# Kernel tuning notes

Hardware: AMD Instinct MI355X
Metric: run time of the kernel (lower is better)

The kernel has to match this reference:

```python
import jax, jax.numpy as jnp
import numpy as np

D = 1024
H = 16
HD = D // H  # 64
HIDDEN = ((int(D * 8 / 3) + 63) // 64) * 64  # 2752
EPS = 1e-6


def rmsnorm(x, w):
    rms = jnp.sqrt(jnp.mean(x * x, axis=-1, keepdims=True) + EPS)
    return x / rms * w


def setup_inputs() -> dict:
    key = jax.random.key(0)
    ks = jax.random.split(key, 12)
    s = lambda fan_in: 1.0 / np.sqrt(fan_in)
    return {
        "x": jax.random.normal(ks[0], (4, 16, 256, D), dtype=jnp.float32),
        "time_emb": jax.random.normal(ks[1], (4, D), dtype=jnp.float32),
        "norm1_w": jnp.ones((D,), dtype=jnp.float32),
        "norm2_w": jnp.ones((D,), dtype=jnp.float32),
        # weights stored (in, out), i.e. transpose of torch nn.Linear.weight
        "qkv_w": jax.random.normal(ks[2], (D, 3 * H * HD), dtype=jnp.float32) * s(D),
        "out_w": jax.random.normal(ks[3], (H * HD, D), dtype=jnp.float32) * s(H * HD),
        "w1": jax.random.normal(ks[4], (D, HIDDEN), dtype=jnp.float32) * s(D),
        "w2": jax.random.normal(ks[5], (D, HIDDEN), dtype=jnp.float32) * s(D),
        "w3": jax.random.normal(ks[6], (HIDDEN, D), dtype=jnp.float32) * s(HIDDEN),
        "mod_w": jax.random.normal(ks[7], (D, 6 * D), dtype=jnp.float32) * s(D),
        "mod_b": jnp.zeros((6 * D,), dtype=jnp.float32),
    }


def spatial_attention(h, qkv_w, out_w):
    # h: (B, T, S, D); attention over S independently per (B, T)
    B, T, S, _ = h.shape
    qkv = jnp.einsum('btsd,de->btse', h, qkv_w)  # (B,T,S,3*H*HD)
    qkv = qkv.reshape(B, T, S, 3, H, HD)
    q, k, v = qkv[..., 0, :, :], qkv[..., 1, :, :], qkv[..., 2, :, :]  # (B,T,S,H,HD)
    scale = HD ** -0.5
    scores = jnp.einsum('btqhd,btkhd->bthqk', q, k) * scale  # (B,T,H,S,S)
    attn = jax.nn.softmax(scores, axis=-1)
    out = jnp.einsum('bthqk,btkhd->btqhd', attn, v).reshape(B, T, S, H * HD)
    return jnp.einsum('btse,ed->btsd', out, out_w)


def reference(x, time_emb, norm1_w, norm2_w, qkv_w, out_w, w1, w2, w3, mod_w, mod_b):
    # adaLN modulation from (B, D) time_emb -> broadcast over (T, S)
    mod = jax.nn.silu(time_emb) @ mod_w + mod_b  # (B, 6D)
    mod = mod[:, None, None, :]  # (B,1,1,6D)
    shift1, scale1, gate1, shift2, scale2, gate2 = jnp.split(mod, 6, axis=-1)

    h = rmsnorm(x, norm1_w) * (1.0 + scale1) + shift1
    h = spatial_attention(h, qkv_w, out_w)
    x = x + gate1 * h

    h = rmsnorm(x, norm2_w) * (1.0 + scale2) + shift2
    h = (jax.nn.silu(h @ w1) * (h @ w2)) @ w3  # SwiGLU
    x = x + gate2 * h
    return x
```

## Files before the change

kernel.cpp:

```cpp
#include <hip/hip_runtime.h>
#include <stdint.h>


using bf16x8 = __attribute__((ext_vector_type(8))) short;
using f32x4  = __attribute__((ext_vector_type(4))) float;

typedef __attribute__((address_space(3))) uint16_t lds16_t;

__device__ __forceinline__ float bf2f(uint16_t h) {
  union { uint32_t u; float f; } v; v.u = ((uint32_t)h) << 16; return v.f;
}
__device__ __forceinline__ uint16_t f2bf(float f) {
  union { float f; uint32_t u; } v; v.f = f;
  uint32_t r = v.u + 0x7FFFu + ((v.u >> 16) & 1u);
  return (uint16_t)(r >> 16);
}
__device__ __forceinline__ float silu(float x) { return x / (1.0f + __expf(-x)); }

__device__ __forceinline__ void gload16(const uint16_t* g, lds16_t* l) {
  __builtin_amdgcn_global_load_lds(
      (const __attribute__((address_space(1))) void*)g,
      (__attribute__((address_space(3))) void*)l, 16, 0, 0);
}

__global__ __launch_bounds__(256)
void transpose_cast(const float* __restrict__ w, uint16_t* __restrict__ wt,
                    int K, int N) {
  __shared__ float tile[32][33];
  int n0 = blockIdx.x * 32, k0 = blockIdx.y * 32;
  int tx = threadIdx.x & 31, ty = threadIdx.x >> 5;
#pragma unroll
  for (int it = 0; it < 4; ++it) {
    int r = ty + it * 8;
    tile[r][tx] = w[(k0 + r) * N + n0 + tx];
  }
  __syncthreads();
#pragma unroll
  for (int it = 0; it < 4; ++it) {
    int r = ty + it * 8;
    wt[(n0 + r) * K + k0 + tx] = f2bf(tile[tx][r]);
  }
}

__global__ __launch_bounds__(1024)
void mod_kernel(const float* __restrict__ te, const float* __restrict__ mw,
                const float* __restrict__ mb, float* __restrict__ mod) {
  __shared__ float ste[4096];
  __shared__ float red[4][4][256];
  int tid = threadIdx.x;
  for (int i = tid; i < 4096; i += 1024) { float v = te[i]; ste[i] = silu(v); }
  __syncthreads();
  int kslice = tid >> 8, cl = tid & 255;
  int col = blockIdx.x * 256 + cl;
  float acc[4] = {0.f, 0.f, 0.f, 0.f};
  for (int kk = 0; kk < 256; ++kk) {
    int k = kslice * 256 + kk;
    float wv = mw[k * 6144 + col];
#pragma unroll
    for (int b = 0; b < 4; ++b) acc[b] += ste[b * 1024 + k] * wv;
  }
#pragma unroll
  for (int b = 0; b < 4; ++b) red[kslice][b][cl] = acc[b];
  __syncthreads();
  if (kslice == 0) {
#pragma unroll
    for (int b = 0; b < 4; ++b)
      mod[b * 6144 + col] =
          red[0][b][cl] + red[1][b][cl] + red[2][b][cl] + red[3][b][cl] + mb[col];
  }
}

__global__ __launch_bounds__(256)
void norm_kernel(const float* __restrict__ xf,
                 const float* __restrict__ w, const float* __restrict__ mod,
                 int shift_off, int scale_off, uint16_t* __restrict__ out) {
  int row = blockIdx.x;
  int b = row >> 12;
  int tid = threadIdx.x;
  float4 t = *(const float4*)(xf + (size_t)row * 1024 + tid * 4);
  float v[4] = {t.x, t.y, t.z, t.w};
  float ss = v[0] * v[0] + v[1] * v[1] + v[2] * v[2] + v[3] * v[3];
#pragma unroll
  for (int off = 1; off < 64; off <<= 1) ss += __shfl_xor(ss, off);
  __shared__ float red[4];
  if ((tid & 63) == 0) red[tid >> 6] = ss;
  __syncthreads();
  float tot = red[0] + red[1] + red[2] + red[3];
  float rinv = rsqrtf(tot * (1.0f / 1024.0f) + 1e-6f);
  const float* mrow = mod + b * 6144;
  uint16_t o[4];
#pragma unroll
  for (int c = 0; c < 4; ++c) {
    int col = tid * 4 + c;
    float hv = v[c] * rinv * w[col] * (1.0f + mrow[scale_off + col]) + mrow[shift_off + col];
    o[c] = f2bf(hv);
  }
  uint2 pk;
  pk.x = (uint32_t)o[0] | ((uint32_t)o[1] << 16);
  pk.y = (uint32_t)o[2] | ((uint32_t)o[3] << 16);
  *(uint2*)(out + (size_t)row * 1024 + tid * 4) = pk;
}

template <int MODE>
__global__ __launch_bounds__(256)
void gemm_bt(const uint16_t* __restrict__ A, const uint16_t* __restrict__ Bt,
             int M, int N, int K,
             uint16_t* __restrict__ obf,
             const float* __restrict__ xin, const float* __restrict__ mod,
             const uint16_t* __restrict__ h1, float* __restrict__ xio) {
  __shared__ uint16_t As[2][128 * 64];
  __shared__ uint16_t Bs[2][128 * 64];
  const int tiles_n = (N + 127) >> 7;
  const int xcd = blockIdx.x & 7;
  const int slot = blockIdx.x >> 3;
  const int tm = (slot / tiles_n) * 8 + xcd;
  const int tn = slot % tiles_n;
  const int m0 = tm * 128, n0 = tn * 128;
  const int tid = threadIdx.x;
  const int wave = tid >> 6, lane = tid & 63;
  const int wm = (wave & 1) * 64, wn = (wave >> 1) * 64;
  const int col = lane & 15, quad = lane >> 4;

  const int srow = tid >> 3, sphys = tid & 7;
  const int slog = ((sphys ^ (srow & 7)) << 3);
  const uint16_t* Ag[4]; const uint16_t* Bg[4];
#pragma unroll
  for (int r = 0; r < 4; ++r) {
    Ag[r] = A + (size_t)(m0 + 32 * r + srow) * K + slog;
    int br = n0 + 32 * r + srow; if (br >= N) br = N - 1;
    Bg[r] = Bt + (size_t)br * K + slog;
  }
  lds16_t* Alb[2]; lds16_t* Blb[2];
#pragma unroll
  for (int b = 0; b < 2; ++b) {
    Alb[b] = (lds16_t*)As[b] + tid * 8;
    Blb[b] = (lds16_t*)Bs[b] + tid * 8;
  }

  f32x4 acc[4][4];
#pragma unroll
  for (int i = 0; i < 4; ++i)
#pragma unroll
    for (int j = 0; j < 4; ++j) acc[i][j] = (f32x4){0.f, 0.f, 0.f, 0.f};

  const int c7 = col & 7;
  const int swzk[2] = {((quad ^ c7) << 3), (((4 + quad) ^ c7) << 3)};

#pragma unroll
  for (int r = 0; r < 4; ++r) gload16(Ag[r], Alb[0] + r * 2048);
#pragma unroll
  for (int r = 0; r < 4; ++r) gload16(Bg[r], Blb[0] + r * 2048);

  for (int k0 = 0; k0 < K; k0 += 64) {
    const int cur = (k0 >> 6) & 1;
    __syncthreads();
    if (k0 + 64 < K) {
      const int kn = k0 + 64;
#pragma unroll
      for (int r = 0; r < 4; ++r) gload16(Ag[r] + kn, Alb[cur ^ 1] + r * 2048);
#pragma unroll
      for (int r = 0; r < 4; ++r) gload16(Bg[r] + kn, Blb[cur ^ 1] + r * 2048);
    }
    const uint16_t* Ab = As[cur];
    const uint16_t* Bb = Bs[cur];
#pragma unroll
    for (int ks = 0; ks < 2; ++ks) {
      const int swz = swzk[ks];
      bf16x8 af[4], bfr[4];
#pragma unroll
      for (int i = 0; i < 4; ++i)
        af[i] = *(const bf16x8*)(Ab + (wm + i * 16 + col) * 64 + swz);
#pragma unroll
      for (int j = 0; j < 4; ++j)
        bfr[j] = *(const bf16x8*)(Bb + (wn + j * 16 + col) * 64 + swz);
#pragma unroll
      for (int i = 0; i < 4; ++i)
#pragma unroll
        for (int j = 0; j < 4; ++j)
          acc[i][j] = __builtin_amdgcn_mfma_f32_16x16x32_bf16(af[i], bfr[j], acc[i][j], 0, 0, 0);
    }
  }

#pragma unroll
  for (int i = 0; i < 4; ++i) {
#pragma unroll
    for (int j = 0; j < 4; ++j) {
#pragma unroll
      for (int r = 0; r < 4; ++r) {
        int row = m0 + wm + i * 16 + quad * 4 + r;
        int cn = n0 + wn + j * 16 + col;
        if (cn >= N) continue;
        float c = acc[i][j][r];
        if (MODE == 0) {
          obf[(size_t)row * N + cn] = f2bf(c);
        } else if (MODE == 1) {
          int b = row >> 12;
          size_t idx = (size_t)row * 1024 + cn;
          float g = mod[b * 6144 + 2048 + cn];
          xio[idx] = xin[idx] + g * c;
        } else if (MODE == 2) {
          obf[(size_t)row * N + cn] = f2bf(silu(c));
        } else if (MODE == 3) {
          size_t idx = (size_t)row * N + cn;
          obf[idx] = f2bf(bf2f(h1[idx]) * c);
        } else {
          int b = row >> 12;
          size_t idx = (size_t)row * 1024 + cn;
          float g = mod[b * 6144 + 5120 + cn];
          xio[idx] = xio[idx] + g * c;
        }
      }
    }
  }
}

__global__ __launch_bounds__(256)
void attn_kernel(const uint16_t* __restrict__ qkv, uint16_t* __restrict__ out) {
  __shared__ uint16_t lds[32768];
  const int tid = threadIdx.x;
  const int bid = blockIdx.x;
  const int slice = bid >> 2, qc = bid & 3;
  const int bt = slice >> 4, h = slice & 15;
  const int row0 = bt * 256;
  const int wave = tid >> 6, lane = tid & 63;
  const int col = lane & 15, quad = lane >> 4;

  {
    int kr = tid;
    const uint16_t* kp = qkv + (size_t)(row0 + kr) * 3072 + 1024 + h * 64;
    uint16_t* ks = lds + kr * 64;
#pragma unroll
    for (int kc = 0; kc < 8; ++kc) {
      uint4 v = *(const uint4*)(kp + kc * 8);
      *(uint4*)(ks + ((kc ^ (kr & 7)) << 3)) = v;
    }
  }
  {
    int p = tid & 127, dh = tid >> 7;
    const uint16_t* vp0 = qkv + (size_t)(row0 + 2 * p) * 3072 + 2048 + h * 64 + dh * 32;
    const uint16_t* vp1 = vp0 + 3072;
    uint16_t r0[32], r1[32];
#pragma unroll
    for (int i = 0; i < 4; ++i) {
      *(uint4*)(r0 + i * 8) = *(const uint4*)(vp0 + i * 8);
      *(uint4*)(r1 + i * 8) = *(const uint4*)(vp1 + i * 8);
    }
    uint32_t* vt = (uint32_t*)(lds + 16384);
    int krc = p >> 2;
#pragma unroll
    for (int i = 0; i < 32; ++i) {
      int d = dh * 32 + i;
      uint32_t val = (uint32_t)r0[i] | ((uint32_t)r1[i] << 16);
      vt[d * 128 + ((krc ^ (d & 7)) << 2) + (p & 3)] = val;
    }
  }
  __syncthreads();

  const int qrow = qc * 64 + wave * 16 + col;
  const uint16_t* qp = qkv + (size_t)(row0 + qrow) * 3072 + h * 64;
  bf16x8 aq0 = *(const bf16x8*)(qp + quad * 8);
  bf16x8 aq1 = *(const bf16x8*)(qp + 32 + quad * 8);

  f32x4 sc[16];
#pragma unroll
  for (int t = 0; t < 16; ++t) {
    int n = t * 16 + col;
    const uint16_t* kb = lds + n * 64;
    bf16x8 b0 = *(const bf16x8*)(kb + ((quad ^ (n & 7)) << 3));
    bf16x8 b1 = *(const bf16x8*)(kb + (((4 + quad) ^ (n & 7)) << 3));
    f32x4 s = (f32x4){0.f, 0.f, 0.f, 0.f};
    s = __builtin_amdgcn_mfma_f32_16x16x32_bf16(aq0, b0, s, 0, 0, 0);
    s = __builtin_amdgcn_mfma_f32_16x16x32_bf16(aq1, b1, s, 0, 0, 0);
    sc[t] = s;
  }

  const float scale = 0.125f;
  float inv[4];
#pragma unroll
  for (int i = 0; i < 4; ++i) {
    float m = -1e30f;
#pragma unroll
    for (int t = 0; t < 16; ++t) m = fmaxf(m, sc[t][i]);
    m = fmaxf(m, __shfl_xor(m, 1));
    m = fmaxf(m, __shfl_xor(m, 2));
    m = fmaxf(m, __shfl_xor(m, 4));
    m = fmaxf(m, __shfl_xor(m, 8));
    m *= scale;
    float sum = 0.f;
#pragma unroll
    for (int t = 0; t < 16; ++t) {
      float p = __expf(sc[t][i] * scale - m);
      sc[t][i] = p;
      sum += p;
    }
    sum += __shfl_xor(sum, 1);
    sum += __shfl_xor(sum, 2);
    sum += __shfl_xor(sum, 4);
    sum += __shfl_xor(sum, 8);
    inv[i] = 1.0f / sum;
  }
  __syncthreads();

  uint16_t* P = lds + wave * 4096;
#pragma unroll
  for (int t = 0; t < 16; ++t) {
    int pcb = t * 2 + (col >> 3);
#pragma unroll
    for (int i = 0; i < 4; ++i) {
      int r = quad * 4 + i;
      P[r * 256 + ((pcb ^ (r & 7)) << 3) + (col & 7)] = f2bf(sc[t][i] * inv[i]);
    }
  }

  f32x4 o[4];
#pragma unroll
  for (int nt = 0; nt < 4; ++nt) o[nt] = (f32x4){0.f, 0.f, 0.f, 0.f};
  const uint16_t* Vt = lds + 16384;
#pragma unroll
  for (int c = 0; c < 8; ++c) {
    int pc = c * 4 + quad;
    bf16x8 ap = *(const bf16x8*)(P + col * 256 + ((pc ^ (col & 7)) << 3));
#pragma unroll
    for (int nt = 0; nt < 4; ++nt) {
      int d = nt * 16 + col;
      bf16x8 bv = *(const bf16x8*)(Vt + d * 256 + ((pc ^ (d & 7)) << 3));
      o[nt] = __builtin_amdgcn_mfma_f32_16x16x32_bf16(ap, bv, o[nt], 0, 0, 0);
    }
  }

#pragma unroll
  for (int nt = 0; nt < 4; ++nt) {
#pragma unroll
    for (int r = 0; r < 4; ++r) {
      int grow = row0 + qc * 64 + wave * 16 + quad * 4 + r;
      int gcol = h * 64 + nt * 16 + col;
      out[(size_t)grow * 1024 + gcol] = f2bf(o[nt][r]);
    }
  }
}

extern "C" void kernel_launch(void* const* d_in, const int* in_sizes, int n_in,
                              void* d_out, int out_size, void* d_ws, size_t ws_size,
                              hipStream_t stream) {
  const float* x        = (const float*)d_in[0];
  const float* time_emb = (const float*)d_in[1];
  const float* norm1_w  = (const float*)d_in[2];
  const float* norm2_w  = (const float*)d_in[3];
  const float* qkv_w    = (const float*)d_in[4];
  const float* out_w    = (const float*)d_in[5];
  const float* w1       = (const float*)d_in[6];
  const float* w2       = (const float*)d_in[7];
  const float* w3       = (const float*)d_in[8];
  const float* mod_w    = (const float*)d_in[9];
  const float* mod_b    = (const float*)d_in[10];
  float* out = (float*)d_out;

  char* ws = (char*)d_ws;
  float*    mod    = (float*)(ws);
  uint16_t* wqkv_t = (uint16_t*)(ws + 98304);
  uint16_t* wout_t = (uint16_t*)(ws + 6389760);
  uint16_t* w1t    = (uint16_t*)(ws + 8486912);
  uint16_t* w2t    = (uint16_t*)(ws + 14123008);
  uint16_t* w3t    = (uint16_t*)(ws + 19759104);
  uint16_t* hbuf   = (uint16_t*)(ws + 25395200);
  uint16_t* qkvb   = (uint16_t*)(ws + 58949632);
  uint16_t* hid    = qkvb;

  dim3 blk(256);
  transpose_cast<<<dim3(3072 / 32, 1024 / 32), blk, 0, stream>>>(qkv_w, wqkv_t, 1024, 3072);
  transpose_cast<<<dim3(1024 / 32, 1024 / 32), blk, 0, stream>>>(out_w, wout_t, 1024, 1024);
  transpose_cast<<<dim3(2752 / 32, 1024 / 32), blk, 0, stream>>>(w1, w1t, 1024, 2752);
  transpose_cast<<<dim3(2752 / 32, 1024 / 32), blk, 0, stream>>>(w2, w2t, 1024, 2752);
  transpose_cast<<<dim3(1024 / 32, 2752 / 32), blk, 0, stream>>>(w3, w3t, 2752, 1024);

  mod_kernel<<<24, 1024, 0, stream>>>(time_emb, mod_w, mod_b, mod);

  norm_kernel<<<16384, blk, 0, stream>>>(x, norm1_w, mod, 0, 1024, hbuf);

  gemm_bt<0><<<128 * 24, blk, 0, stream>>>(hbuf, wqkv_t, 16384, 3072, 1024,
                                           qkvb, nullptr, nullptr, nullptr, nullptr);
  attn_kernel<<<4096, blk, 0, stream>>>(qkvb, hbuf);

  gemm_bt<1><<<128 * 8, blk, 0, stream>>>(hbuf, wout_t, 16384, 1024, 1024,
                                          nullptr, x, mod, nullptr, out);
  norm_kernel<<<16384, blk, 0, stream>>>(out, norm2_w, mod, 3072, 4096, hbuf);

  gemm_bt<2><<<128 * 22, blk, 0, stream>>>(hbuf, w1t, 16384, 2752, 1024,
                                           hid, nullptr, nullptr, nullptr, nullptr);
  gemm_bt<3><<<128 * 22, blk, 0, stream>>>(hbuf, w2t, 16384, 2752, 1024,
                                           hid, nullptr, nullptr, hid, nullptr);
  gemm_bt<4><<<128 * 8, blk, 0, stream>>>(hid, w3t, 16384, 1024, 2752,
                                          nullptr, nullptr, mod, nullptr, out);
}
```

Before: 825.3 us.

## Replace 128x128 GEMM with 256x256-tile 8-wave pipelined GEMM and padded hidden dim

Replaces the 128x128, 4-wave GEMM with a 256x256-tile, 8-wave kernel. Global-to-LDS loads are interleaved between MFMA groups using explicit barriers, waitcnt and setprio scheduling. The SwiGLU hidden dimension is padded from 2752 to 2816, with zero-filled weight buffers, so N and K are multiples of 256/64 and the bounds checks go away. The aim is more data reuse per tile and better overlap of memory and matrix work. The cost is extra memsets, padded compute and heavier register and LDS use per block, which lowers occupancy.

Result: slower. 861.9 us (+4.4%).

```diff
diff --git a/kernel.cpp b/kernel.cpp
--- a/kernel.cpp
+++ b/kernel.cpp
@@ -25,20 +25,20 @@
 
 __global__ __launch_bounds__(256)
 void transpose_cast(const float* __restrict__ w, uint16_t* __restrict__ wt,
-                    int K, int N) {
+                    int K, int N, int ldt) {
   __shared__ float tile[32][33];
   int n0 = blockIdx.x * 32, k0 = blockIdx.y * 32;
   int tx = threadIdx.x & 31, ty = threadIdx.x >> 5;
 #pragma unroll
   for (int it = 0; it < 4; ++it) {
     int r = ty + it * 8;
-    tile[r][tx] = w[(k0 + r) * N + n0 + tx];
+    tile[r][tx] = w[(size_t)(k0 + r) * N + n0 + tx];
   }
   __syncthreads();
 #pragma unroll
   for (int it = 0; it < 4; ++it) {
     int r = ty + it * 8;
-    wt[(n0 + r) * K + k0 + tx] = f2bf(tile[tx][r]);
+    wt[(size_t)(n0 + r) * ldt + k0 + tx] = f2bf(tile[tx][r]);
   }
 }
 
@@ -101,107 +101,161 @@
   *(uint2*)(out + (size_t)row * 1024 + tid * 4) = pk;
 }
 
+
+#define BAR __builtin_amdgcn_s_barrier()
+#define LGKM0                                            \
+  do {                                                   \
+    asm volatile("s_waitcnt lgkmcnt(0)" ::: "memory");   \
+    __builtin_amdgcn_sched_barrier(0);                   \
+  } while (0)
+#define VMW(N) asm volatile("s_waitcnt vmcnt(" #N ")" ::: "memory")
+
+#define GRD4(DST, BASE, ROWB, SWZ)                                           \
+  {                                                                          \
+    _Pragma("unroll") for (int q_ = 0; q_ < 4; ++q_)                         \
+        DST[q_] = *(const bf16x8*)((BASE) + ((ROWB) + q_ * 16 + col) * 64 +  \
+                                   (SWZ));                                   \
+  }
+
+#define MM16(I0, AF)                                                         \
+  {                                                                          \
+    __builtin_amdgcn_s_setprio(1);                                           \
+    _Pragma("unroll") for (int q_ = 0; q_ < 4; ++q_) {                       \
+      _Pragma("unroll") for (int j_ = 0; j_ < 4; ++j_)                       \
+          acc[(I0) + q_][j_] = __builtin_amdgcn_mfma_f32_16x16x32_bf16(      \
+              AF[q_], bf[j_], acc[(I0) + q_][j_], 0, 0, 0);                  \
+    }                                                                        \
+    __builtin_amdgcn_s_setprio(0);                                           \
+  }
+
+#define ADST(S, H, G) ((lds16_t*)As[(S)] + (H) * 8192 + (G) * 4096 + sdoff)
+#define BDST(S, H, G) ((lds16_t*)Bs[(S)] + (H) * 8192 + (G) * 4096 + sdoff)
+
+#define TILE(S, KA, KB, DO_A, DO_B, VMTAIL)                                  \
+  {                                                                          \
+    bf16x8 af[4], bf[4];                                                     \
+                                                                \
+    GRD4(af, As[S], wm * 128, swz0);                                         \
+    GRD4(bf, Bs[S], wn * 64, swz0);                                          \
+    if (DO_A) {                                                              \
+      gload16(aS00 + (KA), ADST((S) ^ 1, 0, 0));                             \
+      gload16(aS01 + (KA), ADST((S) ^ 1, 0, 1));                             \
+    }                                                                        \
+    BAR; LGKM0;                                                              \
+    MM16(0, af);                                                             \
+    BAR;                                                                     \
+                                                                \
+    GRD4(af, As[S], wm * 128 + 64, swz0);                                    \
+    if (DO_A) {                                                              \
+      gload16(aS10 + (KA), ADST((S) ^ 1, 1, 0));                             \
+      gload16(aS11 + (KA), ADST((S) ^ 1, 1, 1));                             \
+    }                                                                        \
+    BAR; LGKM0;                                                              \
+    MM16(4, af);                                                             \
+    BAR;                                                                     \
+                                                                \
+    GRD4(af, As[S], wm * 128, swz1);                                         \
+    GRD4(bf, Bs[S], wn * 64, swz1);                                          \
+    BAR; LGKM0;                                                              \
+    MM16(0, af);                                                             \
+    BAR;                                                                     \
+                                                                \
+    GRD4(af, As[S], wm * 128 + 64, swz1);                                    \
+    if (DO_B) {                                                              \
+      gload16(bS00 + (KB), BDST(S, 0, 0));                                   \
+      gload16(bS01 + (KB), BDST(S, 0, 1));                                   \
+      gload16(bS10 + (KB), BDST(S, 1, 0));                                   \
+      gload16(bS11 + (KB), BDST(S, 1, 1));                                   \
+    }                                                                        \
+    BAR; LGKM0;                                                              \
+    MM16(4, af);                                                             \
+    VMTAIL;                                                                  \
+    BAR;                                                                     \
+  }
+
 template <int MODE>
-__global__ __launch_bounds__(256)
-void gemm_bt(const uint16_t* __restrict__ A, const uint16_t* __restrict__ Bt,
-             int M, int N, int K,
-             uint16_t* __restrict__ obf,
-             const float* __restrict__ xin, const float* __restrict__ mod,
-             const uint16_t* __restrict__ h1, float* __restrict__ xio) {
-  __shared__ uint16_t As[2][128 * 64];
-  __shared__ uint16_t Bs[2][128 * 64];
-  const int tiles_n = (N + 127) >> 7;
+__global__ __launch_bounds__(512)
+void gemm256(const uint16_t* __restrict__ A, int lda,
+             const uint16_t* __restrict__ Bt, int ldb,
+             int N, int K, int ldc,
+             uint16_t* __restrict__ obf, const float* __restrict__ xin,
+             const float* __restrict__ mod, const uint16_t* __restrict__ h1,
+             float* __restrict__ xio) {
+  __shared__ uint16_t As[2][16384];
+  __shared__ uint16_t Bs[2][16384];
+  const int tiles_n = N >> 8;
   const int xcd = blockIdx.x & 7;
-  const int slot = blockIdx.x >> 3;
-  const int tm = (slot / tiles_n) * 8 + xcd;
-  const int tn = slot % tiles_n;
-  const int m0 = tm * 128, n0 = tn * 128;
+  const int bslot = blockIdx.x >> 3;
+  const int tm = (bslot / tiles_n) * 8 + xcd;
+  const int tn = bslot % tiles_n;
+  const int m0 = tm * 256, n0 = tn * 256;
   const int tid = threadIdx.x;
   const int wave = tid >> 6, lane = tid & 63;
-  const int wm = (wave & 1) * 64, wn = (wave >> 1) * 64;
+  const int wm = wave >> 2, wn = wave & 3;
   const int col = lane & 15, quad = lane >> 4;
-
-  const int srow = tid >> 3, sphys = tid & 7;
-  const int slog = ((sphys ^ (srow & 7)) << 3);
-  const uint16_t* Ag[4]; const uint16_t* Bg[4];
-#pragma unroll
-  for (int r = 0; r < 4; ++r) {
-    Ag[r] = A + (size_t)(m0 + 32 * r + srow) * K + slog;
-    int br = n0 + 32 * r + srow; if (br >= N) br = N - 1;
-    Bg[r] = Bt + (size_t)br * K + slog;
-  }
-  lds16_t* Alb[2]; lds16_t* Blb[2];
-#pragma unroll
-  for (int b = 0; b < 2; ++b) {
-    Alb[b] = (lds16_t*)As[b] + tid * 8;
-    Blb[b] = (lds16_t*)Bs[b] + tid * 8;
-  }
-
-  f32x4 acc[4][4];
-#pragma unroll
-  for (int i = 0; i < 4; ++i)
+  const int c7 = col & 7;
+  const int swz0 = (quad ^ c7) << 3;
+  const int swz1 = ((4 + quad) ^ c7) << 3;
+  const int sdoff = wave * 512 + lane * 8;
+
+  const int srl = lane >> 3;
+  const int sl8 = ((lane & 7) ^ srl) << 3;
+  const int rg0 = wave * 8 + srl;
+  const int rg1 = 64 + wave * 8 + srl;
+  const uint16_t* aS00 = A + (size_t)(m0 + rg0) * lda + sl8;
+  const uint16_t* aS01 = A + (size_t)(m0 + rg1) * lda + sl8;
+  const uint16_t* aS10 = A + (size_t)(m0 + 128 + rg0) * lda + sl8;
+  const uint16_t* aS11 = A + (size_t)(m0 + 128 + rg1) * lda + sl8;
+  const uint16_t* bS00 = Bt + (size_t)(n0 + rg0) * ldb + sl8;
+  const uint16_t* bS01 = Bt + (size_t)(n0 + rg1) * ldb + sl8;
+  const uint16_t* bS10 = Bt + (size_t)(n0 + 128 + rg0) * ldb + sl8;
+  const uint16_t* bS11 = Bt + (size_t)(n0 + 128 + rg1) * ldb + sl8;
+
+  f32x4 acc[8][4];
+#pragma unroll
+  for (int i = 0; i < 8; ++i)
 #pragma unroll
     for (int j = 0; j < 4; ++j) acc[i][j] = (f32x4){0.f, 0.f, 0.f, 0.f};
 
-  const int c7 = col & 7;
-  const int swzk[2] = {((quad ^ c7) << 3), (((4 + quad) ^ c7) << 3)};
-
-#pragma unroll
-  for (int r = 0; r < 4; ++r) gload16(Ag[r], Alb[0] + r * 2048);
-#pragma unroll
-  for (int r = 0; r < 4; ++r) gload16(Bg[r], Blb[0] + r * 2048);
-
-  for (int k0 = 0; k0 < K; k0 += 64) {
-    const int cur = (k0 >> 6) & 1;
-    __syncthreads();
-    if (k0 + 64 < K) {
-      const int kn = k0 + 64;
-#pragma unroll
-      for (int r = 0; r < 4; ++r) gload16(Ag[r] + kn, Alb[cur ^ 1] + r * 2048);
-#pragma unroll
-      for (int r = 0; r < 4; ++r) gload16(Bg[r] + kn, Blb[cur ^ 1] + r * 2048);
-    }
-    const uint16_t* Ab = As[cur];
-    const uint16_t* Bb = Bs[cur];
-#pragma unroll
-    for (int ks = 0; ks < 2; ++ks) {
-      const int swz = swzk[ks];
-      bf16x8 af[4], bfr[4];
-#pragma unroll
-      for (int i = 0; i < 4; ++i)
-        af[i] = *(const bf16x8*)(Ab + (wm + i * 16 + col) * 64 + swz);
-#pragma unroll
-      for (int j = 0; j < 4; ++j)
-        bfr[j] = *(const bf16x8*)(Bb + (wn + j * 16 + col) * 64 + swz);
-#pragma unroll
-      for (int i = 0; i < 4; ++i)
-#pragma unroll
-        for (int j = 0; j < 4; ++j)
-          acc[i][j] = __builtin_amdgcn_mfma_f32_16x16x32_bf16(af[i], bfr[j], acc[i][j], 0, 0, 0);
-    }
-  }
-
-#pragma unroll
-  for (int i = 0; i < 4; ++i) {
+  gload16(bS00, BDST(0, 0, 0)); gload16(bS01, BDST(0, 0, 1));
+  gload16(bS10, BDST(0, 1, 0)); gload16(bS11, BDST(0, 1, 1));
+  gload16(aS00, ADST(0, 0, 0)); gload16(aS01, ADST(0, 0, 1));
+  gload16(aS10, ADST(0, 1, 0)); gload16(aS11, ADST(0, 1, 1));
+  gload16(bS00 + 64, BDST(1, 0, 0)); gload16(bS01 + 64, BDST(1, 0, 1));
+  gload16(bS10 + 64, BDST(1, 1, 0)); gload16(bS11 + 64, BDST(1, 1, 1));
+  VMW(4);
+  BAR;
+
+  const int NT = K >> 6;
+  int k0 = 0;
+  for (int t = 0; t + 2 < NT; t += 2) {
+    TILE(0, k0 + 64, k0 + 128, true, true, VMW(4));
+    TILE(1, k0 + 128, k0 + 192, true, true, VMW(4));
+    k0 += 128;
+  }
+  TILE(0, k0 + 64, 0, true, false, VMW(0));
+  TILE(1, 0, 0, false, false, (void)0);
+
+#pragma unroll
+  for (int i = 0; i < 8; ++i) {
 #pragma unroll
     for (int j = 0; j < 4; ++j) {
 #pragma unroll
       for (int r = 0; r < 4; ++r) {
-        int row = m0 + wm + i * 16 + quad * 4 + r;
-        int cn = n0 + wn + j * 16 + col;
-        if (cn >= N) continue;
+        int row = m0 + wm * 128 + i * 16 + quad * 4 + r;
+        int cn = n0 + wn * 64 + j * 16 + col;
         float c = acc[i][j][r];
         if (MODE == 0) {
-          obf[(size_t)row * N + cn] = f2bf(c);
+          obf[(size_t)row * ldc + cn] = f2bf(c);
         } else if (MODE == 1) {
           int b = row >> 12;
           size_t idx = (size_t)row * 1024 + cn;
           float g = mod[b * 6144 + 2048 + cn];
           xio[idx] = xin[idx] + g * c;
         } else if (MODE == 2) {
-          obf[(size_t)row * N + cn] = f2bf(silu(c));
+          obf[(size_t)row * ldc + cn] = f2bf(silu(c));
         } else if (MODE == 3) {
-          size_t idx = (size_t)row * N + cn;
+          size_t idx = (size_t)row * ldc + cn;
           obf[idx] = f2bf(bf2f(h1[idx]) * c);
         } else {
           int b = row >> 12;
@@ -360,35 +414,39 @@
   uint16_t* wqkv_t = (uint16_t*)(ws + 98304);
   uint16_t* wout_t = (uint16_t*)(ws + 6389760);
   uint16_t* w1t    = (uint16_t*)(ws + 8486912);
-  uint16_t* w2t    = (uint16_t*)(ws + 14123008);
-  uint16_t* w3t    = (uint16_t*)(ws + 19759104);
-  uint16_t* hbuf   = (uint16_t*)(ws + 25395200);
-  uint16_t* qkvb   = (uint16_t*)(ws + 58949632);
+  uint16_t* w2t    = (uint16_t*)(ws + 14254080);
+  uint16_t* w3t    = (uint16_t*)(ws + 20021248);
+  uint16_t* hbuf   = (uint16_t*)(ws + 25788416);
+  uint16_t* qkvb   = (uint16_t*)(ws + 59342848);
   uint16_t* hid    = qkvb;
 
+  hipMemsetAsync(w1t, 0, (size_t)2816 * 1024 * 2, stream);
+  hipMemsetAsync(w2t, 0, (size_t)2816 * 1024 * 2, stream);
+  hipMemsetAsync(w3t, 0, (size_t)1024 * 2816 * 2, stream);
+
   dim3 blk(256);
-  transpose_cast<<<dim3(3072 / 32, 1024 / 32), blk, 0, stream>>>(qkv_w, wqkv_t, 1024, 3072);
-  transpose_cast<<<dim3(1024 / 32, 1024 / 32), blk, 0, stream>>>(out_w, wout_t, 1024, 1024);
-  transpose_cast<<<dim3(2752 / 32, 1024 / 32), blk, 0, stream>>>(w1, w1t, 1024, 2752);
-  transpose_cast<<<dim3(2752 / 32, 1024 / 32), blk, 0, stream>>>(w2, w2t, 1024, 2752);
-  transpose_cast<<<dim3(1024 / 32, 2752 / 32), blk, 0, stream>>>(w3, w3t, 2752, 1024);
+  transpose_cast<<<dim3(96, 32), blk, 0, stream>>>(qkv_w, wqkv_t, 1024, 3072, 1024);
+  transpose_cast<<<dim3(32, 32), blk, 0, stream>>>(out_w, wout_t, 1024, 1024, 1024);
+  transpose_cast<<<dim3(86, 32), blk, 0, stream>>>(w1, w1t, 1024, 2752, 1024);
+  transpose_cast<<<dim3(86, 32), blk, 0, stream>>>(w2, w2t, 1024, 2752, 1024);
+  transpose_cast<<<dim3(32, 86), blk, 0, stream>>>(w3, w3t, 2752, 1024, 2816);
 
   mod_kernel<<<24, 1024, 0, stream>>>(time_emb, mod_w, mod_b, mod);
 
   norm_kernel<<<16384, blk, 0, stream>>>(x, norm1_w, mod, 0, 1024, hbuf);
 
-  gemm_bt<0><<<128 * 24, blk, 0, stream>>>(hbuf, wqkv_t, 16384, 3072, 1024,
-                                           qkvb, nullptr, nullptr, nullptr, nullptr);
+  gemm256<0><<<768, 512, 0, stream>>>(hbuf, 1024, wqkv_t, 1024, 3072, 1024, 3072,
+                                      qkvb, nullptr, nullptr, nullptr, nullptr);
   attn_kernel<<<4096, blk, 0, stream>>>(qkvb, hbuf);
 
-  gemm_bt<1><<<128 * 8, blk, 0, stream>>>(hbuf, wout_t, 16384, 1024, 1024,
-                                          nullptr, x, mod, nullptr, out);
+  gemm256<1><<<256, 512, 0, stream>>>(hbuf, 1024, wout_t, 1024, 1024, 1024, 1024,
+                                      nullptr, x, mod, nullptr, out);
   norm_kernel<<<16384, blk, 0, stream>>>(out, norm2_w, mod, 3072, 4096, hbuf);
 
-  gemm_bt<2><<<128 * 22, blk, 0, stream>>>(hbuf, w1t, 16384, 2752, 1024,
-                                           hid, nullptr, nullptr, nullptr, nullptr);
-  gemm_bt<3><<<128 * 22, blk, 0, stream>>>(hbuf, w2t, 16384, 2752, 1024,
-                                           hid, nullptr, nullptr, hid, nullptr);
-  gemm_bt<4><<<128 * 8, blk, 0, stream>>>(hid, w3t, 16384, 1024, 2752,
-                                          nullptr, nullptr, mod, nullptr, out);
-}
+  gemm256<2><<<704, 512, 0, stream>>>(hbuf, 1024, w1t, 1024, 2816, 1024, 2816,
+                                      hid, nullptr, nullptr, nullptr, nullptr);
+  gemm256<3><<<704, 512, 0, stream>>>(hbuf, 1024, w2t, 1024, 2816, 1024, 2816,
+                                      hid, nullptr, nullptr, hid, nullptr);
+  gemm256<4><<<256, 512, 0, stream>>>(hid, 2816, w3t, 2816, 1024, 2816, 1024,
+                                      nullptr, nullptr, mod, nullptr, out);
+}
```
